# Optimization experiments

Measured on AMD Instinct MI355X. Metric: run time of the kernel, lower is better.

Reference implementation:

```python
import jax, jax.numpy as jnp
import numpy as np


def setup_inputs() -> dict:
    key = jax.random.key(0)
    k1, k2, k3, k4 = jax.random.split(key, 4)
    n, L, h = 512, 257, 256
    l = L - 1
    hidden, n_labels = 256, 50
    feat = jax.random.normal(k1, (n, L, h), dtype=jnp.float32)
    heads = jax.random.randint(k2, (n, l), 0, L, dtype=jnp.int64)
    masks = jnp.ones((n, l), dtype=jnp.float32)
    # torch nn.Linear layout: (out_features, in_features); xavier-normal-ish scale
    W1 = jax.random.normal(k3, (hidden, 2 * h), dtype=jnp.float32) * (2.0 / (hidden + 2 * h)) ** 0.5
    b1 = jnp.zeros((hidden,), dtype=jnp.float32)
    W2 = jax.random.normal(k4, (n_labels, hidden), dtype=jnp.float32) * (2.0 / (n_labels + hidden)) ** 0.5
    b2 = jnp.zeros((n_labels,), dtype=jnp.float32)
    return {"feat": feat, "heads": heads, "masks": masks,
            "W1": W1, "b1": b1, "W2": W2, "b2": b2}


def reference(feat, heads, masks, W1, b1, W2, b2):
    # feat: (n, L, h); heads: (n, l) with l = L-1, values in [0, L)
    dependent_f = feat[:, 1:, :]                                   # (n, l, h)
    # head_f[b, i] = feat[b, heads[b, i]]  (the gather)
    head_f = jnp.take_along_axis(feat, heads[:, :, None], axis=1)   # (n, l, h)
    cat_f = jnp.concatenate((dependent_f, head_f), axis=2)          # (n, l, 2h)
    hid = jax.nn.relu(jnp.einsum('nlh,oh->nlo', cat_f, W1) + b1)    # (n, l, hidden); dropout is identity at eval
    label_f = jnp.einsum('nlo,ko->nlk', hid, W2) + b2               # (n, l, n_labels)
    return label_f
```

## Files before the change

kernel.cpp:

```cpp
#include <hip/hip_runtime.h>
#include <hip/hip_bf16.h>
#include <stdint.h>

#define AS1 __attribute__((address_space(1)))
#define AS3 __attribute__((address_space(3)))

typedef __bf16 bf16x8 __attribute__((ext_vector_type(8)));
typedef __bf16 bf16x4 __attribute__((ext_vector_type(4)));
typedef float  floatx4 __attribute__((ext_vector_type(4)));

static constexpr int LL   = 257;
static constexpr int HH   = 256;
static constexpr int M    = 131072;
static constexpr int K1   = 512;
static constexpr int NLAB = 50;

#define MFMA_ACC(ACC, A, B) \
  asm("v_mfma_f32_16x16x32_bf16 %0, %1, %2, %0" : "+a"(ACC) : "v"(A), "v"(B))

template<int IMM>
__device__ __forceinline__ floatx4 gload4i(const float* p) {
  floatx4 v;
  asm volatile("global_load_dwordx4 %0, %1, off offset:%2"
               : "=v"(v) : "v"(p), "i"(IMM) : "memory");
  return v;
}

__device__ __forceinline__ bf16x8 cvt8(floatx4 a, floatx4 b) {
  bf16x8 v;
  v[0]=(__bf16)a[0]; v[1]=(__bf16)a[1]; v[2]=(__bf16)a[2]; v[3]=(__bf16)a[3];
  v[4]=(__bf16)b[0]; v[5]=(__bf16)b[1]; v[6]=(__bf16)b[2]; v[7]=(__bf16)b[3];
  return v;
}

__global__ void prep_w(const float* __restrict__ W1, const float* __restrict__ W2,
                       __bf16* __restrict__ w1bt, __bf16* __restrict__ w2b) {
  int idx = blockIdx.x * 256 + threadIdx.x;
  if (idx < 16384) {
    int o  = idx >> 6;
    int kc = idx & 63;
    const float4* s = (const float4*)(W1 + (size_t)o * K1 + kc * 8);
    float4 a = s[0], b = s[1];
    bf16x8 v;
    v[0]=(__bf16)a.x; v[1]=(__bf16)a.y; v[2]=(__bf16)a.z; v[3]=(__bf16)a.w;
    v[4]=(__bf16)b.x; v[5]=(__bf16)b.y; v[6]=(__bf16)b.z; v[7]=(__bf16)b.w;
    *(bf16x8*)(w1bt + ((size_t)(kc * 256 + o)) * 8) = v;
  } else {
    int j = idx - 16384;
    int row = j >> 5;
    int col = (j & 31) * 8;
    float4 a = {0.f,0.f,0.f,0.f}, b = {0.f,0.f,0.f,0.f};
    if (row < NLAB) {
      const float4* s = (const float4*)(W2 + (size_t)row * 256 + col);
      a = s[0]; b = s[1];
    }
    bf16x8 v;
    v[0]=(__bf16)a.x; v[1]=(__bf16)a.y; v[2]=(__bf16)a.z; v[3]=(__bf16)a.w;
    v[4]=(__bf16)b.x; v[5]=(__bf16)b.y; v[6]=(__bf16)b.z; v[7]=(__bf16)b.w;
    *(bf16x8*)(w2b + (size_t)j * 8) = v;
  }
}

template<int KT>
__device__ __forceinline__ void kstep(
    floatx4 (&catP)[3][4], floatx4 (&afc)[4], floatx4 (&afn)[4],
    floatx4 (&acc)[4][8],
    const float* depP0, const float* depP1,
    const float* headP0, const float* headP1,
    const __bf16* afBase, const __bf16* catS, int bbOff, __bf16* catW0) {

  if constexpr (KT < 15) {
    const __bf16* afp = afBase + (KT + 1) * 8192;
    afn[0] = gload4i<0>((const float*)afp);
    afn[1] = gload4i<256>((const float*)afp);
    afn[2] = gload4i<512>((const float*)afp);
    afn[3] = gload4i<768>((const float*)afp);
  }
  if constexpr (KT <= 12) {
    constexpr int CT  = KT + 3;
    constexpr int OFF = (CT & 7) * 128;
    const float* p0 = (CT < 8) ? depP0 : headP0;
    const float* p1 = (CT < 8) ? depP1 : headP1;
    catP[KT % 3][0] = gload4i<OFF>(p0);
    catP[KT % 3][1] = gload4i<OFF + 16>(p0);
    catP[KT % 3][2] = gload4i<OFF>(p1);
    catP[KT % 3][3] = gload4i<OFF + 16>(p1);
  }

  floatx4 (&cs)[4] = catP[(KT + 1) % 3];
  if constexpr (KT <= 12)
    asm volatile("s_waitcnt vmcnt(12)" : "+v"(afc[0]),"+v"(afc[1]),"+v"(afc[2]),"+v"(afc[3]),
                                         "+v"(cs[0]),"+v"(cs[1]),"+v"(cs[2]),"+v"(cs[3]));
  else if constexpr (KT == 13)
    asm volatile("s_waitcnt vmcnt(8)"  : "+v"(afc[0]),"+v"(afc[1]),"+v"(afc[2]),"+v"(afc[3]),
                                         "+v"(cs[0]),"+v"(cs[1]),"+v"(cs[2]),"+v"(cs[3]));
  else if constexpr (KT == 14)
    asm volatile("s_waitcnt vmcnt(4)"  : "+v"(afc[0]),"+v"(afc[1]),"+v"(afc[2]),"+v"(afc[3]),
                                         "+v"(cs[0]),"+v"(cs[1]),"+v"(cs[2]),"+v"(cs[3]));
  else
    asm volatile("s_waitcnt vmcnt(0)"  : "+v"(afc[0]),"+v"(afc[1]),"+v"(afc[2]),"+v"(afc[3]),
                                         "+v"(cs[0]),"+v"(cs[1]),"+v"(cs[2]),"+v"(cs[3]));

  const __bf16* crd = catS + (KT & 1) * 4096 + bbOff;
  bf16x8 bb[8];
  #pragma unroll
  for (int mi = 0; mi < 8; ++mi)
    bb[mi] = *(const bf16x8*)(crd + mi * 512);
  #pragma unroll
  for (int oi = 0; oi < 4; ++oi) {
    bf16x8 a = __builtin_bit_cast(bf16x8, afc[oi]);
    #pragma unroll
    for (int mi = 0; mi < 8; ++mi)
      MFMA_ACC(acc[oi][mi], a, bb[mi]);
  }

  if constexpr (KT < 15) {
    __bf16* cw = catW0 + ((KT + 1) & 1) * 4096;
    *(bf16x8*)cw          = cvt8(cs[0], cs[1]);
    *(bf16x8*)(cw + 2048) = cvt8(cs[2], cs[3]);
    asm volatile("s_waitcnt lgkmcnt(0)" ::: "memory");
    __builtin_amdgcn_s_barrier();
  }
}

__global__ __launch_bounds__(256, 2)
void fused_kernel(const float* __restrict__ feat, const int* __restrict__ heads,
                  const __bf16* __restrict__ w1bt, const float* __restrict__ b1,
                  const __bf16* __restrict__ w2b, const float* __restrict__ b2,
                  float* __restrict__ out) {
  __shared__ __align__(16) char smem[65536];
  __bf16* catS = (__bf16*)smem;
  __bf16* hidS = (__bf16*)smem;

  const int t    = threadIdx.x;
  const int w    = t >> 6;
  const int lane = t & 63;
  const int lr   = lane & 15;
  const int q    = lane >> 4;
  const int mBase = blockIdx.x * 128;

  const int r0 = t >> 2;
  const int cc = t & 3;
  const int m0 = mBase + r0;
  const int m1 = m0 + 64;
  const int seq = m0 >> 8;
  const float* depP0  = feat + ((size_t)(seq * LL + (m0 & 255) + 1)) * HH + cc * 8;
  const float* depP1  = feat + ((size_t)(seq * LL + (m1 & 255) + 1)) * HH + cc * 8;
  const float* headP0 = feat + ((size_t)(seq * LL + heads[m0])) * HH + cc * 8;
  const float* headP1 = feat + ((size_t)(seq * LL + heads[m1])) * HH + cc * 8;
  asm volatile("" : "+v"(headP0), "+v"(headP1));

  const int pos0 = r0 * 4 + (cc ^ ((r0 >> 1) & 3));
  __bf16* catW0 = catS + pos0 * 8;
  const int bbOff = lr * 32 + (q ^ ((lr >> 1) & 3)) * 8;
  const __bf16* afBase = w1bt + ((size_t)(q * 256 + w * 64 + lr)) * 8;

  floatx4 acc[4][8];
  #pragma unroll
  for (int i = 0; i < 4; ++i)
    #pragma unroll
    for (int j = 0; j < 8; ++j)
      acc[i][j] = (floatx4){0.f, 0.f, 0.f, 0.f};

  floatx4 catP[3][4];
  floatx4 afA[4], afB[4];

  catP[0][0] = gload4i<0>(depP0);    catP[0][1] = gload4i<16>(depP0);
  catP[0][2] = gload4i<0>(depP1);    catP[0][3] = gload4i<16>(depP1);
  catP[1][0] = gload4i<128>(depP0);  catP[1][1] = gload4i<144>(depP0);
  catP[1][2] = gload4i<128>(depP1);  catP[1][3] = gload4i<144>(depP1);
  afA[0] = gload4i<0>((const float*)afBase);
  afA[1] = gload4i<256>((const float*)afBase);
  afA[2] = gload4i<512>((const float*)afBase);
  afA[3] = gload4i<768>((const float*)afBase);
  catP[2][0] = gload4i<256>(depP0);  catP[2][1] = gload4i<272>(depP0);
  catP[2][2] = gload4i<256>(depP1);  catP[2][3] = gload4i<272>(depP1);
  asm volatile("s_waitcnt vmcnt(12)" : "+v"(catP[0][0]),"+v"(catP[0][1]),"+v"(catP[0][2]),"+v"(catP[0][3]));
  *(bf16x8*)catW0          = cvt8(catP[0][0], catP[0][1]);
  *(bf16x8*)(catW0 + 2048) = cvt8(catP[0][2], catP[0][3]);
  asm volatile("s_waitcnt lgkmcnt(0)" ::: "memory");
  __builtin_amdgcn_s_barrier();

  kstep< 0>(catP, afA, afB, acc, depP0, depP1, headP0, headP1, afBase, catS, bbOff, catW0);
  kstep< 1>(catP, afB, afA, acc, depP0, depP1, headP0, headP1, afBase, catS, bbOff, catW0);
  kstep< 2>(catP, afA, afB, acc, depP0, depP1, headP0, headP1, afBase, catS, bbOff, catW0);
  kstep< 3>(catP, afB, afA, acc, depP0, depP1, headP0, headP1, afBase, catS, bbOff, catW0);
  kstep< 4>(catP, afA, afB, acc, depP0, depP1, headP0, headP1, afBase, catS, bbOff, catW0);
  kstep< 5>(catP, afB, afA, acc, depP0, depP1, headP0, headP1, afBase, catS, bbOff, catW0);
  kstep< 6>(catP, afA, afB, acc, depP0, depP1, headP0, headP1, afBase, catS, bbOff, catW0);
  kstep< 7>(catP, afB, afA, acc, depP0, depP1, headP0, headP1, afBase, catS, bbOff, catW0);
  kstep< 8>(catP, afA, afB, acc, depP0, depP1, headP0, headP1, afBase, catS, bbOff, catW0);
  kstep< 9>(catP, afB, afA, acc, depP0, depP1, headP0, headP1, afBase, catS, bbOff, catW0);
  kstep<10>(catP, afA, afB, acc, depP0, depP1, headP0, headP1, afBase, catS, bbOff, catW0);
  kstep<11>(catP, afB, afA, acc, depP0, depP1, headP0, headP1, afBase, catS, bbOff, catW0);
  kstep<12>(catP, afA, afB, acc, depP0, depP1, headP0, headP1, afBase, catS, bbOff, catW0);
  kstep<13>(catP, afB, afA, acc, depP0, depP1, headP0, headP1, afBase, catS, bbOff, catW0);
  kstep<14>(catP, afA, afB, acc, depP0, depP1, headP0, headP1, afBase, catS, bbOff, catW0);
  kstep<15>(catP, afB, afA, acc, depP0, depP1, headP0, headP1, afBase, catS, bbOff, catW0);

  __syncthreads();

  bf16x8 w2f[8];
  #pragma unroll
  for (int kt2 = 0; kt2 < 8; ++kt2)
    w2f[kt2] = *(const bf16x8*)(w2b + (size_t)(w * 16 + lr) * 256 + kt2 * 32 + q * 8);

  float4 biasv[4];
  #pragma unroll
  for (int oi = 0; oi < 4; ++oi)
    biasv[oi] = *(const float4*)(b1 + w * 64 + oi * 16 + q * 4);

  #pragma unroll
  for (int mi = 0; mi < 8; ++mi) {
    const int mr = mi * 16 + lr;
    const int s  = lr & 7;
    #pragma unroll
    for (int oi = 0; oi < 4; ++oi) {
      const int cj = w * 8 + oi * 2 + (q >> 1);
      bf16x4 hv;
      const float* bp = (const float*)&biasv[oi];
      #pragma unroll
      for (int rr = 0; rr < 4; ++rr) {
        float v = acc[oi][mi][rr] + bp[rr];
        v = v > 0.f ? v : 0.f;
        hv[rr] = (__bf16)v;
      }
      *(bf16x4*)(hidS + mr * 256 + ((cj ^ s) << 3) + (q & 1) * 4) = hv;
    }
  }
  __syncthreads();

  floatx4 acc2[8];
  #pragma unroll
  for (int i = 0; i < 8; ++i) acc2[i] = (floatx4){0.f, 0.f, 0.f, 0.f};

  #pragma unroll
  for (int kt2 = 0; kt2 < 8; ++kt2) {
    const int gc = kt2 * 4 + q;
    #pragma unroll
    for (int mi = 0; mi < 8; ++mi) {
      bf16x8 a2 = *(const bf16x8*)(hidS + (mi * 16 + lr) * 256 + ((gc ^ (lr & 7)) << 3));
      acc2[mi] = __builtin_amdgcn_mfma_f32_16x16x32_bf16(a2, w2f[kt2], acc2[mi], 0, 0, 0);
    }
  }
  __syncthreads();

  float* outT = (float*)smem;
  const int col = w * 16 + lr;
  if (col < NLAB) {
    const float bias = b2[col];
    #pragma unroll
    for (int mi = 0; mi < 8; ++mi) {
      const int rowB = mi * 16 + q * 4;
      #pragma unroll
      for (int rr = 0; rr < 4; ++rr)
        outT[(rowB + rr) * NLAB + col] = acc2[mi][rr] + bias;
    }
  }
  __syncthreads();

  float* odst = out + (size_t)mBase * NLAB;
  #pragma unroll
  for (int i = t; i < 1600; i += 256)
    *(float4*)(odst + i * 4) = *(const float4*)(outT + i * 4);
}

extern "C" void kernel_launch(void* const* d_in, const int* in_sizes, int n_in,
                              void* d_out, int out_size, void* d_ws, size_t ws_size,
                              hipStream_t stream) {
  const float* feat  = (const float*)d_in[0];
  const int*   heads = (const int*)d_in[1];
  const float* W1 = (const float*)d_in[3];
  const float* b1 = (const float*)d_in[4];
  const float* W2 = (const float*)d_in[5];
  const float* b2 = (const float*)d_in[6];
  float* out = (float*)d_out;

  __bf16* w1bt = (__bf16*)d_ws;
  __bf16* w2b  = w1bt + 256 * 512;

  prep_w<<<72, 256, 0, stream>>>(W1, W2, w1bt, w2b);
  fused_kernel<<<M / 128, 256, 0, stream>>>(feat, heads, w1bt, b1, w2b, b2, out);
}
```

Before: 231.9 us.

## Halve the row tile to 64 rows per block and shrink shared memory

New measurement: 239.0 us. +3.1%, slower.

```diff
diff --git a/kernel.cpp b/kernel.cpp
--- a/kernel.cpp
+++ b/kernel.cpp
@@ -63,10 +63,9 @@
 
 template<int KT>
 __device__ __forceinline__ void kstep(
-    floatx4 (&catP)[3][4], floatx4 (&afc)[4], floatx4 (&afn)[4],
-    floatx4 (&acc)[4][8],
-    const float* depP0, const float* depP1,
-    const float* headP0, const float* headP1,
+    floatx4 (&catP)[3][2], floatx4 (&afc)[4], floatx4 (&afn)[4],
+    floatx4 (&acc)[4][4],
+    const float* depP, const float* headP,
     const __bf16* afBase, const __bf16* catS, int bbOff, __bf16* catW0) {
 
   if constexpr (KT < 15) {
@@ -79,47 +78,45 @@
   if constexpr (KT <= 12) {
     constexpr int CT  = KT + 3;
     constexpr int OFF = (CT & 7) * 128;
-    const float* p0 = (CT < 8) ? depP0 : headP0;
-    const float* p1 = (CT < 8) ? depP1 : headP1;
-    catP[KT % 3][0] = gload4i<OFF>(p0);
-    catP[KT % 3][1] = gload4i<OFF + 16>(p0);
-    catP[KT % 3][2] = gload4i<OFF>(p1);
-    catP[KT % 3][3] = gload4i<OFF + 16>(p1);
-  }
-
-  floatx4 (&cs)[4] = catP[(KT + 1) % 3];
+    const float* p = (CT < 8) ? depP : headP;
+    catP[KT % 3][0] = gload4i<OFF>(p);
+    catP[KT % 3][1] = gload4i<OFF + 16>(p);
+  }
+
+  floatx4 (&cs)[2] = catP[(KT + 1) % 3];
   if constexpr (KT <= 12)
-    asm volatile("s_waitcnt vmcnt(12)" : "+v"(afc[0]),"+v"(afc[1]),"+v"(afc[2]),"+v"(afc[3]),
-                                         "+v"(cs[0]),"+v"(cs[1]),"+v"(cs[2]),"+v"(cs[3]));
+    asm volatile("s_waitcnt vmcnt(8)" : "+v"(afc[0]),"+v"(afc[1]),"+v"(afc[2]),"+v"(afc[3]),
+                                        "+v"(cs[0]),"+v"(cs[1]));
   else if constexpr (KT == 13)
-    asm volatile("s_waitcnt vmcnt(8)"  : "+v"(afc[0]),"+v"(afc[1]),"+v"(afc[2]),"+v"(afc[3]),
-                                         "+v"(cs[0]),"+v"(cs[1]),"+v"(cs[2]),"+v"(cs[3]));
+    asm volatile("s_waitcnt vmcnt(6)" : "+v"(afc[0]),"+v"(afc[1]),"+v"(afc[2]),"+v"(afc[3]),
+                                        "+v"(cs[0]),"+v"(cs[1]));
   else if constexpr (KT == 14)
-    asm volatile("s_waitcnt vmcnt(4)"  : "+v"(afc[0]),"+v"(afc[1]),"+v"(afc[2]),"+v"(afc[3]),
-                                         "+v"(cs[0]),"+v"(cs[1]),"+v"(cs[2]),"+v"(cs[3]));
+    asm volatile("s_waitcnt vmcnt(4)" : "+v"(afc[0]),"+v"(afc[1]),"+v"(afc[2]),"+v"(afc[3]),
+                                        "+v"(cs[0]),"+v"(cs[1]));
   else
     asm volatile("s_waitcnt vmcnt(0)"  : "+v"(afc[0]),"+v"(afc[1]),"+v"(afc[2]),"+v"(afc[3]),
-                                         "+v"(cs[0]),"+v"(cs[1]),"+v"(cs[2]),"+v"(cs[3]));
-
-  const __bf16* crd = catS + (KT & 1) * 4096 + bbOff;
-  bf16x8 bb[8];
-  #pragma unroll
-  for (int mi = 0; mi < 8; ++mi)
+                                         "+v"(cs[0]),"+v"(cs[1]));
+
+  const __bf16* crd = catS + (KT & 1) * 2048 + bbOff;
+  bf16x8 bb[4];
+  #pragma unroll
+  for (int mi = 0; mi < 4; ++mi)
     bb[mi] = *(const bf16x8*)(crd + mi * 512);
   #pragma unroll
   for (int oi = 0; oi < 4; ++oi) {
     bf16x8 a = __builtin_bit_cast(bf16x8, afc[oi]);
     #pragma unroll
-    for (int mi = 0; mi < 8; ++mi)
+    for (int mi = 0; mi < 4; ++mi)
       MFMA_ACC(acc[oi][mi], a, bb[mi]);
   }
 
   if constexpr (KT < 15) {
-    __bf16* cw = catW0 + ((KT + 1) & 1) * 4096;
-    *(bf16x8*)cw          = cvt8(cs[0], cs[1]);
-    *(bf16x8*)(cw + 2048) = cvt8(cs[2], cs[3]);
+    __bf16* cw = catW0 + ((KT + 1) & 1) * 2048;
+    *(bf16x8*)cw = cvt8(cs[0], cs[1]);
+    __builtin_amdgcn_sched_barrier(0);
     asm volatile("s_waitcnt lgkmcnt(0)" ::: "memory");
     __builtin_amdgcn_s_barrier();
+    __builtin_amdgcn_sched_barrier(0);
   }
 }
 
@@ -128,7 +125,7 @@
                   const __bf16* __restrict__ w1bt, const float* __restrict__ b1,
                   const __bf16* __restrict__ w2b, const float* __restrict__ b2,
                   float* __restrict__ out) {
-  __shared__ __align__(16) char smem[65536];
+  __shared__ __align__(16) char smem[32768];
   __bf16* catS = (__bf16*)smem;
   __bf16* hidS = (__bf16*)smem;
 
@@ -137,73 +134,63 @@
   const int lane = t & 63;
   const int lr   = lane & 15;
   const int q    = lane >> 4;
-  const int mBase = blockIdx.x * 128;
-
-  const int r0 = t >> 2;
-  const int cc = t & 3;
-  const int m0 = mBase + r0;
-  const int m1 = m0 + 64;
+  const int mBase = blockIdx.x * 64;
+
+  const int r = t >> 2;
+  const int c = t & 3;
+  const int m0 = mBase + r;
   const int seq = m0 >> 8;
-  const float* depP0  = feat + ((size_t)(seq * LL + (m0 & 255) + 1)) * HH + cc * 8;
-  const float* depP1  = feat + ((size_t)(seq * LL + (m1 & 255) + 1)) * HH + cc * 8;
-  const float* headP0 = feat + ((size_t)(seq * LL + heads[m0])) * HH + cc * 8;
-  const float* headP1 = feat + ((size_t)(seq * LL + heads[m1])) * HH + cc * 8;
-  asm volatile("" : "+v"(headP0), "+v"(headP1));
-
-  const int pos0 = r0 * 4 + (cc ^ ((r0 >> 1) & 3));
+  const float* depP  = feat + ((size_t)(seq * LL + (m0 & 255) + 1)) * HH + c * 8;
+  const float* headP = feat + ((size_t)(seq * LL + heads[m0])) * HH + c * 8;
+  asm volatile("" : "+v"(headP));
+
+  const int pos0 = r * 4 + (c ^ ((r >> 1) & 3));
   __bf16* catW0 = catS + pos0 * 8;
   const int bbOff = lr * 32 + (q ^ ((lr >> 1) & 3)) * 8;
   const __bf16* afBase = w1bt + ((size_t)(q * 256 + w * 64 + lr)) * 8;
 
-  floatx4 acc[4][8];
+  floatx4 acc[4][4];
   #pragma unroll
   for (int i = 0; i < 4; ++i)
     #pragma unroll
-    for (int j = 0; j < 8; ++j)
+    for (int j = 0; j < 4; ++j)
       acc[i][j] = (floatx4){0.f, 0.f, 0.f, 0.f};
 
-  floatx4 catP[3][4];
+  floatx4 catP[3][2];
   floatx4 afA[4], afB[4];
 
-  catP[0][0] = gload4i<0>(depP0);    catP[0][1] = gload4i<16>(depP0);
-  catP[0][2] = gload4i<0>(depP1);    catP[0][3] = gload4i<16>(depP1);
-  catP[1][0] = gload4i<128>(depP0);  catP[1][1] = gload4i<144>(depP0);
-  catP[1][2] = gload4i<128>(depP1);  catP[1][3] = gload4i<144>(depP1);
+  catP[0][0] = gload4i<0>(depP);    catP[0][1] = gload4i<16>(depP);
+  catP[1][0] = gload4i<128>(depP);  catP[1][1] = gload4i<144>(depP);
   afA[0] = gload4i<0>((const float*)afBase);
   afA[1] = gload4i<256>((const float*)afBase);
   afA[2] = gload4i<512>((const float*)afBase);
   afA[3] = gload4i<768>((const float*)afBase);
-  catP[2][0] = gload4i<256>(depP0);  catP[2][1] = gload4i<272>(depP0);
-  catP[2][2] = gload4i<256>(depP1);  catP[2][3] = gload4i<272>(depP1);
-  asm volatile("s_waitcnt vmcnt(12)" : "+v"(catP[0][0]),"+v"(catP[0][1]),"+v"(catP[0][2]),"+v"(catP[0][3]));
-  *(bf16x8*)catW0          = cvt8(catP[0][0], catP[0][1]);
-  *(bf16x8*)(catW0 + 2048) = cvt8(catP[0][2], catP[0][3]);
+  catP[2][0] = gload4i<256>(depP);  catP[2][1] = gload4i<272>(depP);
+  asm volatile("s_waitcnt vmcnt(8)" : "+v"(catP[0][0]),"+v"(catP[0][1]));
+  *(bf16x8*)catW0 = cvt8(catP[0][0], catP[0][1]);
+  __builtin_amdgcn_sched_barrier(0);
   asm volatile("s_waitcnt lgkmcnt(0)" ::: "memory");
   __builtin_amdgcn_s_barrier();
-
-  kstep< 0>(catP, afA, afB, acc, depP0, depP1, headP0, headP1, afBase, catS, bbOff, catW0);
-  kstep< 1>(catP, afB, afA, acc, depP0, depP1, headP0, headP1, afBase, catS, bbOff, catW0);
-  kstep< 2>(catP, afA, afB, acc, depP0, depP1, headP0, headP1, afBase, catS, bbOff, catW0);
-  kstep< 3>(catP, afB, afA, acc, depP0, depP1, headP0, headP1, afBase, catS, bbOff, catW0);
-  kstep< 4>(catP, afA, afB, acc, depP0, depP1, headP0, headP1, afBase, catS, bbOff, catW0);
-  kstep< 5>(catP, afB, afA, acc, depP0, depP1, headP0, headP1, afBase, catS, bbOff, catW0);
-  kstep< 6>(catP, afA, afB, acc, depP0, depP1, headP0, headP1, afBase, catS, bbOff, catW0);
-  kstep< 7>(catP, afB, afA, acc, depP0, depP1, headP0, headP1, afBase, catS, bbOff, catW0);
-  kstep< 8>(catP, afA, afB, acc, depP0, depP1, headP0, headP1, afBase, catS, bbOff, catW0);
-  kstep< 9>(catP, afB, afA, acc, depP0, depP1, headP0, headP1, afBase, catS, bbOff, catW0);
-  kstep<10>(catP, afA, afB, acc, depP0, depP1, headP0, headP1, afBase, catS, bbOff, catW0);
-  kstep<11>(catP, afB, afA, acc, depP0, depP1, headP0, headP1, afBase, catS, bbOff, catW0);
-  kstep<12>(catP, afA, afB, acc, depP0, depP1, headP0, headP1, afBase, catS, bbOff, catW0);
-  kstep<13>(catP, afB, afA, acc, depP0, depP1, headP0, headP1, afBase, catS, bbOff, catW0);
-  kstep<14>(catP, afA, afB, acc, depP0, depP1, headP0, headP1, afBase, catS, bbOff, catW0);
-  kstep<15>(catP, afB, afA, acc, depP0, depP1, headP0, headP1, afBase, catS, bbOff, catW0);
-
-  __syncthreads();
-
-  bf16x8 w2f[8];
-  #pragma unroll
-  for (int kt2 = 0; kt2 < 8; ++kt2)
-    w2f[kt2] = *(const bf16x8*)(w2b + (size_t)(w * 16 + lr) * 256 + kt2 * 32 + q * 8);
+  __builtin_amdgcn_sched_barrier(0);
+
+  kstep< 0>(catP, afA, afB, acc, depP, headP, afBase, catS, bbOff, catW0);
+  kstep< 1>(catP, afB, afA, acc, depP, headP, afBase, catS, bbOff, catW0);
+  kstep< 2>(catP, afA, afB, acc, depP, headP, afBase, catS, bbOff, catW0);
+  kstep< 3>(catP, afB, afA, acc, depP, headP, afBase, catS, bbOff, catW0);
+  kstep< 4>(catP, afA, afB, acc, depP, headP, afBase, catS, bbOff, catW0);
+  kstep< 5>(catP, afB, afA, acc, depP, headP, afBase, catS, bbOff, catW0);
+  kstep< 6>(catP, afA, afB, acc, depP, headP, afBase, catS, bbOff, catW0);
+  kstep< 7>(catP, afB, afA, acc, depP, headP, afBase, catS, bbOff, catW0);
+  kstep< 8>(catP, afA, afB, acc, depP, headP, afBase, catS, bbOff, catW0);
+  kstep< 9>(catP, afB, afA, acc, depP, headP, afBase, catS, bbOff, catW0);
+  kstep<10>(catP, afA, afB, acc, depP, headP, afBase, catS, bbOff, catW0);
+  kstep<11>(catP, afB, afA, acc, depP, headP, afBase, catS, bbOff, catW0);
+  kstep<12>(catP, afA, afB, acc, depP, headP, afBase, catS, bbOff, catW0);
+  kstep<13>(catP, afB, afA, acc, depP, headP, afBase, catS, bbOff, catW0);
+  kstep<14>(catP, afA, afB, acc, depP, headP, afBase, catS, bbOff, catW0);
+  kstep<15>(catP, afB, afA, acc, depP, headP, afBase, catS, bbOff, catW0);
+
+  __syncthreads();
 
   float4 biasv[4];
   #pragma unroll
@@ -211,7 +198,7 @@
     biasv[oi] = *(const float4*)(b1 + w * 64 + oi * 16 + q * 4);
 
   #pragma unroll
-  for (int mi = 0; mi < 8; ++mi) {
+  for (int mi = 0; mi < 4; ++mi) {
     const int mr = mi * 16 + lr;
     const int s  = lr & 7;
     #pragma unroll
@@ -230,15 +217,20 @@
   }
   __syncthreads();
 
-  floatx4 acc2[8];
-  #pragma unroll
-  for (int i = 0; i < 8; ++i) acc2[i] = (floatx4){0.f, 0.f, 0.f, 0.f};
+  bf16x8 w2f[8];
+  #pragma unroll
+  for (int kt2 = 0; kt2 < 8; ++kt2)
+    w2f[kt2] = *(const bf16x8*)(w2b + (size_t)(w * 16 + lr) * 256 + kt2 * 32 + q * 8);
+
+  floatx4 acc2[4];
+  #pragma unroll
+  for (int i = 0; i < 4; ++i) acc2[i] = (floatx4){0.f, 0.f, 0.f, 0.f};
 
   #pragma unroll
   for (int kt2 = 0; kt2 < 8; ++kt2) {
     const int gc = kt2 * 4 + q;
     #pragma unroll
-    for (int mi = 0; mi < 8; ++mi) {
+    for (int mi = 0; mi < 4; ++mi) {
       bf16x8 a2 = *(const bf16x8*)(hidS + (mi * 16 + lr) * 256 + ((gc ^ (lr & 7)) << 3));
       acc2[mi] = __builtin_amdgcn_mfma_f32_16x16x32_bf16(a2, w2f[kt2], acc2[mi], 0, 0, 0);
     }
@@ -250,7 +242,7 @@
   if (col < NLAB) {
     const float bias = b2[col];
     #pragma unroll
-    for (int mi = 0; mi < 8; ++mi) {
+    for (int mi = 0; mi < 4; ++mi) {
       const int rowB = mi * 16 + q * 4;
       #pragma unroll
       for (int rr = 0; rr < 4; ++rr)
@@ -261,7 +253,7 @@
 
   float* odst = out + (size_t)mBase * NLAB;
   #pragma unroll
-  for (int i = t; i < 1600; i += 256)
+  for (int i = t; i < 800; i += 256)
     *(float4*)(odst + i * 4) = *(const float4*)(outT + i * 4);
 }
 
@@ -280,5 +272,5 @@
   __bf16* w2b  = w1bt + 256 * 512;
 
   prep_w<<<72, 256, 0, stream>>>(W1, W2, w1bt, w2b);
-  fused_kernel<<<M / 128, 256, 0, stream>>>(feat, heads, w1bt, b1, w2b, b2, out);
-}
+  fused_kernel<<<M / 64, 256, 0, stream>>>(feat, heads, w1bt, b1, w2b, b2, out);
+}
```
